# Kernel optimization log

Hardware: AMD Instinct MI355X
Metric: run time of the kernel (lower is better)

## Reference

```python
import jax, jax.numpy as jnp
import numpy as np

NNODES = 16384
DIM = 512
ALPHA = 3.0
K = 10  # min(scale_hyperedges=10, nnodes)


def setup_inputs() -> dict:
    key = jax.random.key(0)
    k1, k2, k3 = jax.random.split(key, 3)
    return {
        "idx": jnp.arange(NNODES, dtype=jnp.int32),
        # nn.Embedding default init: N(0, 1)
        "emb_weight": jax.random.normal(k1, (NNODES, DIM), dtype=jnp.float32),
        # nn.Linear default init scale ~ 1/sqrt(fan_in)
        "lin_w": jax.random.uniform(k2, (DIM, DIM), dtype=jnp.float32,
                                    minval=-1.0, maxval=1.0) / np.float32(np.sqrt(DIM)),
        "lin_b": jax.random.uniform(k3, (DIM,), dtype=jnp.float32,
                                    minval=-1.0, maxval=1.0) / np.float32(np.sqrt(DIM)),
    }


def reference(idx, emb_weight, lin_w, lin_b):
    # node_features = emb1(idx)                      [N, D]
    feats = emb_weight[idx]
    # transformed = tanh(alpha * lin1(feats))        [N, D]
    t = jnp.tanh(ALPHA * (feats @ lin_w.T + lin_b))
    # sim = T @ T^T                                  [N, N]
    sim = t @ t.T
    # top-k most similar nodes per row
    _, top_idx = jax.lax.top_k(sim, K)               # [N, K]
    n = emb_weight.shape[0]
    rows = jnp.arange(n)[:, None]                    # [N, 1]
    # H[i, top_idx[i]] = 1, then transpose -> incidence [nodes, hyperedges]
    H = jnp.zeros((n, n), dtype=t.dtype).at[rows, top_idx].set(1.0)
    return H.T
```

## Files before the change

### kernel.cpp

```cpp
#include <hip/hip_runtime.h>
#include <hip/hip_bf16.h>
#include <math.h>

#define NN 16384
#define DD 512
#define KSEL 10
#define MCAND 16
#define NSPLIT 4
#define RESCORE 16

typedef __bf16 bf16x8 __attribute__((ext_vector_type(8)));
typedef float  f32x4  __attribute__((ext_vector_type(4)));

#define GLOAD_LDS16(gsrc, ldst) \
    __builtin_amdgcn_global_load_lds( \
        (const __attribute__((address_space(1))) void*)(gsrc), \
        (__attribute__((address_space(3))) void*)(ldst), 16, 0, 0)

__global__ __launch_bounds__(256) void k_transform(
    const int* __restrict__ idx, const float* __restrict__ emb,
    const float* __restrict__ W, const float* __restrict__ bias,
    float* __restrict__ t_out, unsigned short* __restrict__ tb_out)
{
    __shared__ float As[32][68];
    __shared__ float Bs[32][68];
    const int tid = threadIdx.x;
    const int tx = tid & 15, ty = tid >> 4;
    const int m0 = (blockIdx.x >> 3) << 6;
    const int n0 = (blockIdx.x & 7) << 6;

    float acc[4][4] = {};

    const int f0 = tid, f1 = tid + 256;
    const int r0 = f0 >> 3, c0_ = f0 & 7;
    const int r1 = f1 >> 3, c1_ = f1 & 7;
    const int ga0 = idx[m0 + r0];
    const int ga1 = idx[m0 + r1];

    for (int kc = 0; kc < DD; kc += 32) {
        const float4 a0 = *(const float4*)&emb[(size_t)ga0 * DD + kc + (c0_ << 2)];
        const float4 a1 = *(const float4*)&emb[(size_t)ga1 * DD + kc + (c1_ << 2)];
        const float4 b0 = *(const float4*)&W[(size_t)(n0 + r0) * DD + kc + (c0_ << 2)];
        const float4 b1 = *(const float4*)&W[(size_t)(n0 + r1) * DD + kc + (c1_ << 2)];
        As[(c0_<<2)+0][r0] = a0.x; As[(c0_<<2)+1][r0] = a0.y;
        As[(c0_<<2)+2][r0] = a0.z; As[(c0_<<2)+3][r0] = a0.w;
        As[(c1_<<2)+0][r1] = a1.x; As[(c1_<<2)+1][r1] = a1.y;
        As[(c1_<<2)+2][r1] = a1.z; As[(c1_<<2)+3][r1] = a1.w;
        Bs[(c0_<<2)+0][r0] = b0.x; Bs[(c0_<<2)+1][r0] = b0.y;
        Bs[(c0_<<2)+2][r0] = b0.z; Bs[(c0_<<2)+3][r0] = b0.w;
        Bs[(c1_<<2)+0][r1] = b1.x; Bs[(c1_<<2)+1][r1] = b1.y;
        Bs[(c1_<<2)+2][r1] = b1.z; Bs[(c1_<<2)+3][r1] = b1.w;
        __syncthreads();
        #pragma unroll
        for (int k = 0; k < 32; ++k) {
            const float4 a = *(const float4*)&As[k][ty << 2];
            const float4 b = *(const float4*)&Bs[k][tx << 2];
            const float av[4] = {a.x, a.y, a.z, a.w};
            const float bv[4] = {b.x, b.y, b.z, b.w};
            #pragma unroll
            for (int i = 0; i < 4; ++i)
                #pragma unroll
                for (int j = 0; j < 4; ++j)
                    acc[i][j] = fmaf(av[i], bv[j], acc[i][j]);
        }
        __syncthreads();
    }

    #pragma unroll
    for (int i = 0; i < 4; ++i) {
        const int m = m0 + (ty << 2) + i;
        float o[4];
        union { __hip_bfloat16 h[4]; ushort4 u; } cc;
        #pragma unroll
        for (int j = 0; j < 4; ++j) {
            const int n = n0 + (tx << 2) + j;
            o[j] = tanhf(3.0f * (acc[i][j] + bias[n]));
            cc.h[j] = __float2bfloat16(o[j]);
        }
        *(float4*)&t_out[(size_t)m * DD + n0 + (tx << 2)] =
            make_float4(o[0], o[1], o[2], o[3]);
        *(ushort4*)&tb_out[(size_t)m * DD + n0 + (tx << 2)] = cc.u;
    }
}

__global__ __launch_bounds__(512) void k_sim_topk(
    const unsigned short* __restrict__ tb,
    float* __restrict__ pv, unsigned short* __restrict__ pi)
{
    __shared__ __align__(16) char SM[124928];
    unsigned short* Ab0 = (unsigned short*)(SM);
    unsigned short* Ab1 = (unsigned short*)(SM + 32768);
    unsigned short* Bb0 = (unsigned short*)(SM + 65536);
    unsigned short* Bb1 = (unsigned short*)(SM + 81920);
    float*          topv   = (float*)(SM + 98304);
    unsigned short* topi   = (unsigned short*)(SM + 114688);
    float*          thresh = (float*)(SM + 122880);
    int*            cnt    = (int*)(SM + 123904);
    float*          cv     = (float*)(SM);
    unsigned short* ci     = (unsigned short*)(SM + 32768);

    const int tid  = threadIdx.x;
    const int wave = tid >> 6;
    const int lane = tid & 63;
    const int wr   = wave >> 1;
    const int wc   = wave & 1;

    const int bid  = blockIdx.x;
    const int s    = (bid & 7) >> 1;
    const int mblk = ((bid & 1) << 5) | (bid >> 3);
    const int m0   = mblk << 8;
    const int c_begin = s * (NN / NSPLIT);

    if (tid < 256) {
        thresh[tid] = -1e30f;
        cnt[tid] = 0;
        #pragma unroll
        for (int j = 0; j < MCAND; ++j) { topv[tid*MCAND + j] = -1e30f; topi[tid*MCAND + j] = 0xFFFFu; }
    }
    __syncthreads();

    const int lr8 = lane >> 3;
    const int scx = ((lane & 7) ^ lr8) << 4;
    const char* tbb = (const char*)tb;

#define STAGE_STEP(Ad, Bd, kb) do { \
    _Pragma("unroll") \
    for (int i_ = 0; i_ < 4; ++i_) { \
        const int ai_ = (wave << 2) + i_; \
        GLOAD_LDS16(tbb + (size_t)(m0 + (ai_ << 3) + lr8) * 1024 + (kb) + scx, \
                    (char*)(Ad) + (ai_ << 10)); \
    } \
    _Pragma("unroll") \
    for (int i_ = 0; i_ < 2; ++i_) { \
        const int bi_ = (wave << 1) + i_; \
        GLOAD_LDS16(tbb + (size_t)(c0 + (bi_ << 3) + lr8) * 1024 + (kb) + scx, \
                    (char*)(Bd) + (bi_ << 10)); \
    } \
} while (0)

    for (int ct = 0; ct < (NN / NSPLIT) / 128; ++ct) {
        const int c0 = c_begin + (ct << 7);
        f32x4 acc[4][4] = {};

        STAGE_STEP(Ab0, Bb0, 0);
        __syncthreads();

        for (int kc8 = 0; kc8 < 8; ++kc8) {
            const int par = kc8 & 1;
            if (kc8 < 7) {
                const size_t kb = (size_t)((kc8 + 1) << 7);
                if (par == 0) { STAGE_STEP(Ab1, Bb1, kb); }
                else          { STAGE_STEP(Ab0, Bb0, kb); }
            }
            const unsigned short* Ac = par ? Ab1 : Ab0;
            const unsigned short* Bc = par ? Bb1 : Bb0;
            #pragma unroll
            for (int ks = 0; ks < 2; ++ks) {
                bf16x8 af[4], bf[4];
                #pragma unroll
                for (int m = 0; m < 4; ++m) {
                    const int row = (wr << 6) + (m << 4) + (lane & 15);
                    const int corig = (ks << 2) + (lane >> 4);
                    af[m] = *(const bf16x8*)((const char*)Ac +
                            (row << 7) + ((corig ^ (row & 7)) << 4));
                }
                #pragma unroll
                for (int n = 0; n < 4; ++n) {
                    const int row = (wc << 6) + (n << 4) + (lane & 15);
                    const int corig = (ks << 2) + (lane >> 4);
                    bf[n] = *(const bf16x8*)((const char*)Bc +
                            (row << 7) + ((corig ^ (row & 7)) << 4));
                }
                #pragma unroll
                for (int m = 0; m < 4; ++m)
                    #pragma unroll
                    for (int n = 0; n < 4; ++n)
                        acc[m][n] = __builtin_amdgcn_mfma_f32_16x16x32_bf16(
                            af[m], bf[n], acc[m][n], 0, 0, 0);
            }
            __syncthreads();
        }

        #pragma unroll
        for (int rnd = 0; rnd < 4; ++rnd) {
            const int wcr = rnd >> 1;
            const int nf0 = (rnd & 1) << 1;
            if (wc == wcr) {
                #pragma unroll
                for (int m = 0; m < 4; ++m) {
                    #pragma unroll
                    for (int nn = 0; nn < 2; ++nn) {
                        #pragma unroll
                        for (int j = 0; j < 4; ++j) {
                            const int row = (wr << 6) + (m << 4) + ((lane >> 4) << 2) + j;
                            const float v = acc[m][nf0 + nn][j];
                            if (v >= thresh[row]) {
                                const int p = atomicAdd(&cnt[row], 1);
                                cv[(row << 5) + p] = v;
                                ci[(row << 5) + p] =
                                    (unsigned short)(c0 + (wcr << 6) + ((nf0 + nn) << 4) + (lane & 15));
                            }
                        }
                    }
                }
            }
            __syncthreads();
            if (tid < 256) {
                const int r = tid;
                const int n_ = cnt[r];
                float* tv = &topv[r * MCAND];
                unsigned short* ti = &topi[r * MCAND];
                for (int q = 0; q < n_; ++q) {
                    const float v = cv[(r << 5) + q];
                    const unsigned short c = ci[(r << 5) + q];
                    if (v > tv[MCAND-1] || (v == tv[MCAND-1] && c < ti[MCAND-1])) {
                        int p = MCAND - 1;
                        while (p > 0 && (v > tv[p-1] || (v == tv[p-1] && c < ti[p-1]))) {
                            tv[p] = tv[p-1]; ti[p] = ti[p-1]; --p;
                        }
                        tv[p] = v; ti[p] = c;
                    }
                }
                cnt[r] = 0;
                thresh[r] = tv[MCAND-1];
            }
            __syncthreads();
        }
    }
#undef STAGE_STEP

    if (tid < 256) {
        const size_t base = (((size_t)s * 64 + mblk) * 256 + tid) * MCAND;
        #pragma unroll
        for (int j = 0; j < MCAND; ++j) {
            pv[base + j] = topv[tid * MCAND + j];
            pi[base + j] = topi[tid * MCAND + j];
        }
    }
}

__global__ __launch_bounds__(256) void k_rescore(
    const float* __restrict__ t, const float* __restrict__ pv,
    const unsigned short* __restrict__ pi, float* __restrict__ out)
{
    const int wave = threadIdx.x >> 6;
    const int lane = threadIdx.x & 63;
    const int r = blockIdx.x * 4 + wave;
    const int mblk = r >> 8, local = r & 255;

    const int sp = lane >> 4, slot = lane & 15;
    const size_t cbase = (((size_t)sp * 64 + mblk) * 256 + local) * MCAND;
    const float v = pv[cbase + slot];
    const unsigned int idxc = pi[cbase + slot];
    const unsigned int u = __float_as_uint(v);
    const unsigned int mkey = (u & 0x80000000u) ? ~u : (u | 0x80000000u);
    unsigned long long key = ((unsigned long long)mkey << 16) |
                             (unsigned long long)((~idxc) & 0xFFFFu);

    #pragma unroll
    for (int k = 2; k <= 64; k <<= 1) {
        #pragma unroll
        for (int j = k >> 1; j > 0; j >>= 1) {
            const unsigned long long other = __shfl_xor(key, j, 64);
            const bool lower = (lane & j) == 0;
            const bool ascBlock = (lane & k) == 0;
            const bool takeMax = (lower == ascBlock);
            const bool mineBigger = key > other;
            key = (takeMax == mineBigger) ? key : other;
        }
    }
    const int cid = (int)((~(unsigned int)key) & 0xFFFFu);

    const float4 a0 = *(const float4*)&t[(size_t)r * DD + lane * 8];
    const float4 a1 = *(const float4*)&t[(size_t)r * DD + lane * 8 + 4];

    double bestv[KSEL];
    int    besti[KSEL];
    #pragma unroll
    for (int j = 0; j < KSEL; ++j) { bestv[j] = -1e300; besti[j] = 0x7fffffff; }

    for (int q = 0; q < RESCORE; ++q) {
        const int c = __shfl(cid, q, 64);
        const float4 v0 = *(const float4*)&t[(size_t)c * DD + lane * 8];
        const float4 v1 = *(const float4*)&t[(size_t)c * DD + lane * 8 + 4];
        double sdot = 0.0;
        sdot += (double)a0.x * (double)v0.x;
        sdot += (double)a0.y * (double)v0.y;
        sdot += (double)a0.z * (double)v0.z;
        sdot += (double)a0.w * (double)v0.w;
        sdot += (double)a1.x * (double)v1.x;
        sdot += (double)a1.y * (double)v1.y;
        sdot += (double)a1.z * (double)v1.z;
        sdot += (double)a1.w * (double)v1.w;
        #pragma unroll
        for (int off = 32; off > 0; off >>= 1)
            sdot += __shfl_down(sdot, off, 64);
        if (lane == 0) {
            if (sdot > bestv[KSEL-1] || (sdot == bestv[KSEL-1] && c < besti[KSEL-1])) {
                int p = KSEL - 1;
                while (p > 0 && (sdot > bestv[p-1] ||
                                 (sdot == bestv[p-1] && c < besti[p-1]))) {
                    bestv[p] = bestv[p-1]; besti[p] = besti[p-1]; --p;
                }
                bestv[p] = sdot; besti[p] = c;
            }
        }
    }

    if (lane == 0) {
        #pragma unroll
        for (int j = 0; j < KSEL; ++j)
            out[(size_t)besti[j] * NN + r] = 1.0f;
    }
}

extern "C" void kernel_launch(void* const* d_in, const int* in_sizes, int n_in,
                              void* d_out, int out_size, void* d_ws, size_t ws_size,
                              hipStream_t stream) {
    const int*   idx  = (const int*)d_in[0];
    const float* emb  = (const float*)d_in[1];
    const float* linw = (const float*)d_in[2];
    const float* linb = (const float*)d_in[3];
    float* out = (float*)d_out;

    float*          t  = (float*)d_ws;
    unsigned short* tb = (unsigned short*)((char*)d_ws + (size_t)32 * 1024 * 1024);
    float*          pv = (float*)((char*)d_ws + (size_t)48 * 1024 * 1024);
    unsigned short* pi = (unsigned short*)((char*)d_ws + (size_t)52 * 1024 * 1024);

    (void)hipMemsetAsync(d_out, 0, (size_t)NN * (size_t)NN * sizeof(float), stream);

    k_transform<<<dim3(256 * 8), dim3(256), 0, stream>>>(idx, emb, linw, linb, t, tb);
    k_sim_topk<<<dim3(256), dim3(512), 0, stream>>>(tb, pv, pi);
    k_rescore<<<dim3(NN / 4), dim3(256), 0, stream>>>(t, pv, pi, out);
}
```

Before: 2.338 ms.

## Use 4-stage K pipeline with 64-wide chunks and fine-grained vmcnt waits

Replaces the double-buffered 128-element K staging with a four-buffer ring of 64-element K chunks, prefetching two chunks ahead and using s_waitcnt vmcnt plus a raw s_barrier instead of a full __syncthreads per step. The LDS swizzle is adapted to 64-byte rows. The aim is to keep more global loads in flight so they overlap MFMA work, and to cut barrier overhead in the sim GEMM. The candidate buffers are also re-padded to a stride of 33 with int indices to reduce LDS bank conflicts in the top-k merge. Ring reuse safety rests on the barrier ordering and on the vmcnt counts matching the three loads issued per stage.

```diff
diff --git a/kernel.cpp b/kernel.cpp
--- a/kernel.cpp
+++ b/kernel.cpp
@@ -88,16 +88,12 @@
     float* __restrict__ pv, unsigned short* __restrict__ pi)
 {
     __shared__ __align__(16) char SM[124928];
-    unsigned short* Ab0 = (unsigned short*)(SM);
-    unsigned short* Ab1 = (unsigned short*)(SM + 32768);
-    unsigned short* Bb0 = (unsigned short*)(SM + 65536);
-    unsigned short* Bb1 = (unsigned short*)(SM + 81920);
     float*          topv   = (float*)(SM + 98304);
     unsigned short* topi   = (unsigned short*)(SM + 114688);
     float*          thresh = (float*)(SM + 122880);
     int*            cnt    = (int*)(SM + 123904);
     float*          cv     = (float*)(SM);
-    unsigned short* ci     = (unsigned short*)(SM + 32768);
+    int*            ci     = (int*)(SM + 36864);
 
     const int tid  = threadIdx.x;
     const int wave = tid >> 6;
@@ -119,67 +115,71 @@
     }
     __syncthreads();
 
-    const int lr8 = lane >> 3;
-    const int scx = ((lane & 7) ^ lr8) << 4;
     const char* tbb = (const char*)tb;
-
-#define STAGE_STEP(Ad, Bd, kb) do { \
-    _Pragma("unroll") \
-    for (int i_ = 0; i_ < 4; ++i_) { \
-        const int ai_ = (wave << 2) + i_; \
-        GLOAD_LDS16(tbb + (size_t)(m0 + (ai_ << 3) + lr8) * 1024 + (kb) + scx, \
-                    (char*)(Ad) + (ai_ << 10)); \
-    } \
-    _Pragma("unroll") \
-    for (int i_ = 0; i_ < 2; ++i_) { \
-        const int bi_ = (wave << 1) + i_; \
-        GLOAD_LDS16(tbb + (size_t)(c0 + (bi_ << 3) + lr8) * 1024 + (kb) + scx, \
-                    (char*)(Bd) + (bi_ << 10)); \
-    } \
-} while (0)
+    const int l4r = lane >> 2;
+    const int l4u = lane & 3;
 
     for (int ct = 0; ct < (NN / NSPLIT) / 128; ++ct) {
         const int c0 = c_begin + (ct << 7);
         f32x4 acc[4][4] = {};
 
-        STAGE_STEP(Ab0, Bb0, 0);
+        auto STAGE = [&](int k) {
+            const int rb = k & 3;
+            const size_t kb = (size_t)k << 6;
+            char* Ad = SM + (rb << 14);
+            char* Bd = SM + 65536 + (rb << 13);
+            #pragma unroll
+            for (int i_ = 0; i_ < 2; ++i_) {
+                const int rl = (wave << 5) + (i_ << 4) + l4r;
+                GLOAD_LDS16(tbb + (size_t)(m0 + rl) * 1024 + kb + ((size_t)(l4u ^ ((rl >> 1) & 3)) << 4),
+                            Ad + (wave << 11) + (i_ << 10));
+            }
+            {
+                const int rl = (wave << 4) + l4r;
+                GLOAD_LDS16(tbb + (size_t)(c0 + rl) * 1024 + kb + ((size_t)(l4u ^ ((rl >> 1) & 3)) << 4),
+                            Bd + (wave << 10));
+            }
+        };
+
+        auto COMPUTE = [&](int k) {
+            const int rb = k & 3;
+            const char* Ac = SM + (rb << 14);
+            const char* Bc = SM + 65536 + (rb << 13);
+            const int u = lane >> 4;
+            bf16x8 af[4], bf[4];
+            #pragma unroll
+            for (int m = 0; m < 4; ++m) {
+                const int row = (wr << 6) + (m << 4) + (lane & 15);
+                af[m] = *(const bf16x8*)(Ac + (row << 6) + ((u ^ ((row >> 1) & 3)) << 4));
+            }
+            #pragma unroll
+            for (int n = 0; n < 4; ++n) {
+                const int row = (wc << 6) + (n << 4) + (lane & 15);
+                bf[n] = *(const bf16x8*)(Bc + (row << 6) + ((u ^ ((row >> 1) & 3)) << 4));
+            }
+            #pragma unroll
+            for (int m = 0; m < 4; ++m)
+                #pragma unroll
+                for (int n = 0; n < 4; ++n)
+                    acc[m][n] = __builtin_amdgcn_mfma_f32_16x16x32_bf16(
+                        af[m], bf[n], acc[m][n], 0, 0, 0);
+        };
+
+        STAGE(0); STAGE(1);
+        for (int kc = 0; kc < 14; ++kc) {
+            asm volatile("s_waitcnt vmcnt(3)" ::: "memory");
+            __builtin_amdgcn_s_barrier();
+            STAGE(kc + 2);
+            COMPUTE(kc);
+        }
+        asm volatile("s_waitcnt vmcnt(3)" ::: "memory");
+        __builtin_amdgcn_s_barrier();
+        COMPUTE(14);
+        asm volatile("s_waitcnt vmcnt(0)" ::: "memory");
+        __builtin_amdgcn_s_barrier();
+        COMPUTE(15);
+
         __syncthreads();
-
-        for (int kc8 = 0; kc8 < 8; ++kc8) {
-            const int par = kc8 & 1;
-            if (kc8 < 7) {
-                const size_t kb = (size_t)((kc8 + 1) << 7);
-                if (par == 0) { STAGE_STEP(Ab1, Bb1, kb); }
-                else          { STAGE_STEP(Ab0, Bb0, kb); }
-            }
-            const unsigned short* Ac = par ? Ab1 : Ab0;
-            const unsigned short* Bc = par ? Bb1 : Bb0;
-            #pragma unroll
-            for (int ks = 0; ks < 2; ++ks) {
-                bf16x8 af[4], bf[4];
-                #pragma unroll
-                for (int m = 0; m < 4; ++m) {
-                    const int row = (wr << 6) + (m << 4) + (lane & 15);
-                    const int corig = (ks << 2) + (lane >> 4);
-                    af[m] = *(const bf16x8*)((const char*)Ac +
-                            (row << 7) + ((corig ^ (row & 7)) << 4));
-                }
-                #pragma unroll
-                for (int n = 0; n < 4; ++n) {
-                    const int row = (wc << 6) + (n << 4) + (lane & 15);
-                    const int corig = (ks << 2) + (lane >> 4);
-                    bf[n] = *(const bf16x8*)((const char*)Bc +
-                            (row << 7) + ((corig ^ (row & 7)) << 4));
-                }
-                #pragma unroll
-                for (int m = 0; m < 4; ++m)
-                    #pragma unroll
-                    for (int n = 0; n < 4; ++n)
-                        acc[m][n] = __builtin_amdgcn_mfma_f32_16x16x32_bf16(
-                            af[m], bf[n], acc[m][n], 0, 0, 0);
-            }
-            __syncthreads();
-        }
 
         #pragma unroll
         for (int rnd = 0; rnd < 4; ++rnd) {
@@ -196,9 +196,8 @@
                             const float v = acc[m][nf0 + nn][j];
                             if (v >= thresh[row]) {
                                 const int p = atomicAdd(&cnt[row], 1);
-                                cv[(row << 5) + p] = v;
-                                ci[(row << 5) + p] =
-                                    (unsigned short)(c0 + (wcr << 6) + ((nf0 + nn) << 4) + (lane & 15));
+                                cv[row * 33 + p] = v;
+                                ci[row * 33 + p] = c0 + (wcr << 6) + ((nf0 + nn) << 4) + (lane & 15);
                             }
                         }
                     }
@@ -211,8 +210,8 @@
                 float* tv = &topv[r * MCAND];
                 unsigned short* ti = &topi[r * MCAND];
                 for (int q = 0; q < n_; ++q) {
-                    const float v = cv[(r << 5) + q];
-                    const unsigned short c = ci[(r << 5) + q];
+                    const float v = cv[r * 33 + q];
+                    const unsigned short c = (unsigned short)ci[r * 33 + q];
                     if (v > tv[MCAND-1] || (v == tv[MCAND-1] && c < ti[MCAND-1])) {
                         int p = MCAND - 1;
                         while (p > 0 && (v > tv[p-1] || (v == tv[p-1] && c < ti[p-1]))) {
@@ -227,7 +226,6 @@
             __syncthreads();
         }
     }
-#undef STAGE_STEP
 
     if (tid < 256) {
         const size_t base = (((size_t)s * 64 + mblk) * 256 + tid) * MCAND;
```

Result: no change. 2.321 ms (-0.7%).
